# Optimization experiments

Measured on AMD Instinct MI355X. Metric: run time of the kernel, lower is better.

Reference implementation:

```python
import jax, jax.numpy as jnp
import numpy as np

SEQ, EMBED, H, QLR, KVLR, RD, VD = 4096, 2048, 16, 512, 512, 64, 128
KD = VD + RD  # full key/query head dim (content + rope)


def _make_rotary_pe(seq_len, dim):
    inv_freq = 1.0 / jnp.power(10000.0, jnp.arange(0, dim, 2) / dim)
    t = jnp.arange(seq_len)
    freqs = jnp.outer(t, inv_freq)  # (seq, dim//2)
    return jnp.sin(freqs), jnp.cos(freqs)


def _apply_rope(x, sin, cos):
    # x: (seq, ..., dim); sin/cos: (seq, dim//2)
    d = x.shape[-1] // 2
    x1, x2 = x[..., :d], x[..., d:]
    sin2 = jnp.concatenate([sin, sin], axis=-1)
    cos2 = jnp.concatenate([cos, cos], axis=-1)
    ne = x.ndim - 2
    sin2 = sin2.reshape(sin2.shape[0], *[1] * ne, sin2.shape[1])
    cos2 = cos2.reshape(cos2.shape[0], *[1] * ne, cos2.shape[1])
    rot = jnp.concatenate([-x2, x1], axis=-1)
    return x * cos2 + rot * sin2


def setup_inputs() -> dict:
    key = jax.random.key(0)
    ks = jax.random.split(key, 8)

    def w(k, out_dim, in_dim):
        return jax.random.normal(k, (out_dim, in_dim), dtype=jnp.float32) * (1.0 / np.sqrt(in_dim))

    x = jax.random.normal(ks[0], (SEQ, EMBED), dtype=jnp.float32)
    mask = jnp.tril(jnp.ones((SEQ, SEQ), dtype=bool))  # causal
    return {
        "x": x,
        "mask": mask,
        "w_q_down": w(ks[1], QLR, EMBED),
        "w_q_up": w(ks[2], H * VD, QLR),
        "w_q_rope": w(ks[3], H * RD, QLR),
        "w_kv_down": w(ks[4], KVLR, EMBED),
        "w_kv_up": w(ks[5], H * 2 * VD, KVLR),
        "w_k_rope": w(ks[6], RD, EMBED),
        "w_out": w(ks[7], EMBED, H * VD),
    }


def reference(x, mask, w_q_down, w_q_up, w_q_rope, w_kv_down, w_kv_up, w_k_rope, w_out):
    seq = x.shape[0]
    # query path through low-rank bottleneck
    c_q = x @ w_q_down.T                                   # (S, QLR)
    q_content = (c_q @ w_q_up.T).reshape(seq, H, VD)       # (S, H, VD)
    q_rope = (c_q @ w_q_rope.T).reshape(seq, H, RD)        # (S, H, RD)
    # kv path through shared low-rank bottleneck
    c_kv = x @ w_kv_down.T                                 # (S, KVLR)
    kv = c_kv @ w_kv_up.T                                  # (S, H*2*VD)
    k_content_flat, v_flat = jnp.split(kv, 2, axis=-1)
    k_content = k_content_flat.reshape(seq, H, VD)
    v = v_flat.reshape(seq, H, VD)
    # shared rope key (one per token, broadcast to heads)
    k_rope_shared = (x @ w_k_rope.T)[:, None, :]           # (S, 1, RD)
    sin, cos = _make_rotary_pe(seq, RD)
    q_rope_rot = _apply_rope(q_rope, sin, cos)             # (S, H, RD)
    k_rope_rot = jnp.tile(_apply_rope(k_rope_shared, sin, cos), (1, H, 1))
    q_final = jnp.concatenate([q_content, q_rope_rot], axis=-1)  # (S, H, KD)
    k_final = jnp.concatenate([k_content, k_rope_rot], axis=-1)  # (S, H, KD)
    # values zero-padded to key dim
    v_padded = jnp.concatenate(
        [v, jnp.zeros((seq, H, RD), dtype=v.dtype)], axis=-1)    # (S, H, KD)
    # scaled dot-product attention per head
    scale = 1.0 / jnp.sqrt(jnp.asarray(KD, dtype=x.dtype))
    scores = jnp.einsum("shd,thd->hst", q_final, k_final) * scale  # (H, S, S)
    scores = jnp.where(mask[None, :, :], scores, jnp.asarray(-1e9, dtype=scores.dtype))
    probs = jax.nn.softmax(scores, axis=-1)
    attn = jnp.einsum("hst,thd->shd", probs, v_padded)             # (S, H, KD)
    attn = attn[..., :VD].reshape(seq, H * VD)                     # drop zero-pad dims
    return attn @ w_out.T                                          # (S, EMBED)
```

## Files before the change

### kernel.cpp

```cpp
#include <hip/hip_runtime.h>


#define SEQ   4096
#define EMBED 2048
#define NHEAD 16
#define QLR   512
#define KVLR  512
#define RD    64
#define VD    128
#define KDIM  192

typedef __attribute__((ext_vector_type(8)))  _Float16 half8;
typedef __attribute__((ext_vector_type(4)))  _Float16 half4;
typedef __attribute__((ext_vector_type(4)))  float    f32x4;
typedef __attribute__((ext_vector_type(16))) float    f32x16;
typedef __attribute__((ext_vector_type(2)))  unsigned int uint2v;
typedef __attribute__((ext_vector_type(4)))  unsigned int uint4v;

__device__ __forceinline__ void gload16(void* lds, const void* g) {
    __builtin_amdgcn_global_load_lds(
        (const __attribute__((address_space(1))) void*)g,
        (__attribute__((address_space(3))) void*)lds, 16, 0, 0);
}

__device__ __forceinline__ unsigned int pkh(float a, float b) {
    auto h = __builtin_amdgcn_cvt_pkrtz(a, b);
    return __builtin_bit_cast(unsigned int, h);
}

__global__ __launch_bounds__(256) void cvt_plain(const float* __restrict__ s,
                                                 _Float16* __restrict__ d, int n8) {
    const int i = blockIdx.x * 256 + threadIdx.x;
    if (i >= n8) return;
    const float4 a = reinterpret_cast<const float4*>(s)[i * 2];
    const float4 b = reinterpret_cast<const float4*>(s)[i * 2 + 1];
    half8 r;
    r[0] = (_Float16)a.x; r[1] = (_Float16)a.y; r[2] = (_Float16)a.z; r[3] = (_Float16)a.w;
    r[4] = (_Float16)b.x; r[5] = (_Float16)b.y; r[6] = (_Float16)b.z; r[7] = (_Float16)b.w;
    reinterpret_cast<half8*>(d)[i] = r;
}

__global__ __launch_bounds__(256) void cvt_down(const float* __restrict__ wqd,
                                                const float* __restrict__ wkvd,
                                                const float* __restrict__ wkr,
                                                _Float16* __restrict__ dst) {
    const int i = blockIdx.x * 256 + threadIdx.x;
    if (i >= 1152 * 2048 / 8) return;
    const int e = i * 8, row = e >> 11, col = e & 2047;
    const float* src = row < 512  ? wqd  + (size_t)row * 2048 + col
                     : row < 1024 ? wkvd + (size_t)(row - 512) * 2048 + col
                     : row < 1088 ? wkr  + (size_t)(row - 1024) * 2048 + col
                                  : nullptr;
    half8 r = {};
    if (src) {
        const float4 a = reinterpret_cast<const float4*>(src)[0];
        const float4 b = reinterpret_cast<const float4*>(src)[1];
        r[0] = (_Float16)a.x; r[1] = (_Float16)a.y; r[2] = (_Float16)a.z; r[3] = (_Float16)a.w;
        r[4] = (_Float16)b.x; r[5] = (_Float16)b.y; r[6] = (_Float16)b.z; r[7] = (_Float16)b.w;
    }
    reinterpret_cast<half8*>(dst)[i] = r;
}

__global__ __launch_bounds__(256) void cvt_qup(const float* __restrict__ wqu,
                                               const float* __restrict__ wqr,
                                               _Float16* __restrict__ dst) {
    const int i = blockIdx.x * 256 + threadIdx.x;
    if (i >= 3072 * 512 / 8) return;
    const int e = i * 8, row = e >> 9, col = e & 511;
    const float* src = row < 2048 ? wqu + (size_t)row * 512 + col
                                  : wqr + (size_t)(row - 2048) * 512 + col;
    const float4 a = reinterpret_cast<const float4*>(src)[0];
    const float4 b = reinterpret_cast<const float4*>(src)[1];
    half8 r;
    r[0] = (_Float16)a.x; r[1] = (_Float16)a.y; r[2] = (_Float16)a.z; r[3] = (_Float16)a.w;
    r[4] = (_Float16)b.x; r[5] = (_Float16)b.y; r[6] = (_Float16)b.z; r[7] = (_Float16)b.w;
    reinterpret_cast<half8*>(dst)[i] = r;
}

template <int EPI>
__global__ __launch_bounds__(256) void gemm_f16(const _Float16* __restrict__ A,
                                                const _Float16* __restrict__ B,
                                                _Float16* __restrict__ o0,
                                                _Float16* __restrict__ o1,
                                                _Float16* __restrict__ o2,
                                                float* __restrict__ of,
                                                int M, int N, int K)
{
    __shared__ _Float16 sA[128 * 64];
    __shared__ _Float16 sB[128 * 64];

    const int tid  = threadIdx.x;
    const int wid  = tid >> 6;
    const int lane = tid & 63;
    const int lr   = lane & 15;
    const int lg   = lane >> 4;
    const int row0 = blockIdx.y * 128;
    const int col0 = blockIdx.x * 128;
    const int war  = (wid >> 1) * 64;
    const int wac  = (wid & 1) * 64;

    const int sr = lane >> 3;
    const int sk = (lane & 7) * 8;
    const _Float16* Ab = A + (size_t)(row0 + wid * 8 + sr) * K + sk;
    const _Float16* Bb = B + (size_t)(col0 + wid * 8 + sr) * K + sk;

    f32x4 acc[4][4] = {};

    for (int k0 = 0; k0 < K; k0 += 64) {
#pragma unroll
        for (int i = 0; i < 4; ++i) {
            const int c = i * 4 + wid;
            gload16((char*)sA + c * 1024, Ab + (size_t)i * 32 * K + k0);
            gload16((char*)sB + c * 1024, Bb + (size_t)i * 32 * K + k0);
        }
        __syncthreads();

#pragma unroll
        for (int kk = 0; kk < 64; kk += 32) {
            half8 a[4], b[4];
#pragma unroll
            for (int i = 0; i < 4; ++i)
                a[i] = *reinterpret_cast<const half8*>(&sA[(war + i * 16 + lr) * 64 + kk + lg * 8]);
#pragma unroll
            for (int j = 0; j < 4; ++j)
                b[j] = *reinterpret_cast<const half8*>(&sB[(wac + j * 16 + lr) * 64 + kk + lg * 8]);
            __builtin_amdgcn_s_setprio(1);
#pragma unroll
            for (int i = 0; i < 4; ++i)
#pragma unroll
                for (int j = 0; j < 4; ++j)
                    acc[i][j] = __builtin_amdgcn_mfma_f32_16x16x32_f16(a[i], b[j], acc[i][j], 0, 0, 0);
            __builtin_amdgcn_s_setprio(0);
        }
        __syncthreads();
    }

#pragma unroll
    for (int i = 0; i < 4; ++i)
#pragma unroll
        for (int j = 0; j < 4; ++j) {
            const int grow0 = row0 + war + i * 16 + lg * 4;
            const int gcol  = col0 + wac + j * 16 + lr;
            if constexpr (EPI == 2) {
                if (gcol >= 2048) {
                    half4 pv;
#pragma unroll
                    for (int r = 0; r < 4; ++r) pv[r] = (_Float16)acc[i][j][r];
                    *reinterpret_cast<half4*>(&o1[(size_t)(gcol - 2048) * SEQ + grow0]) = pv;
                    continue;
                }
            }
#pragma unroll
            for (int r = 0; r < 4; ++r) {
                const int grow = grow0 + r;
                const float v = acc[i][j][r];
                if constexpr (EPI == 0) {
                    if (gcol < 512)       o0[(size_t)grow * 512 + gcol] = (_Float16)v;
                    else if (gcol < 1024) o1[(size_t)grow * 512 + gcol - 512] = (_Float16)v;
                    else if (gcol < 1088) o2[(size_t)grow * 64 + gcol - 1024] = (_Float16)v;
                } else if constexpr (EPI == 1) {
                    if (gcol < 2048)
                        o0[(size_t)grow * (NHEAD * KDIM) + (gcol >> 7) * KDIM + (gcol & 127)] = (_Float16)v;
                    else {
                        const int c = gcol - 2048;
                        o0[(size_t)grow * (NHEAD * KDIM) + (c >> 6) * KDIM + VD + (c & 63)] = (_Float16)v;
                    }
                } else if constexpr (EPI == 2) {
                    o0[((size_t)(gcol >> 7) * SEQ + grow) * KDIM + (gcol & 127)] = (_Float16)v;
                } else {
                    of[(size_t)grow * N + gcol] = v;
                }
            }
        }
}

__global__ __launch_bounds__(256) void rope_kernel(_Float16* __restrict__ qf,
                                                   _Float16* __restrict__ kf,
                                                   const _Float16* __restrict__ ktmp)
{
    __shared__ float s_sin[32], s_cos[32];
    const int s   = blockIdx.x;
    const int tid = threadIdx.x;
    if (tid < 32) {
        const double inv = exp(-(double)tid * (log(10000.0) / 32.0));
        const double ang = (double)s * inv;
        s_sin[tid] = (float)sin(ang);
        s_cos[tid] = (float)cos(ang);
    }
    __syncthreads();

    for (int p = tid; p < NHEAD * 32; p += 256) {
        const int h = p >> 5, i = p & 31;
        const size_t base = (size_t)s * (NHEAD * KDIM) + h * KDIM + VD;
        const float x1 = (float)qf[base + i];
        const float x2 = (float)qf[base + 32 + i];
        const float cs = s_cos[i], sn = s_sin[i];
        qf[base + i]      = (_Float16)(x1 * cs - x2 * sn);
        qf[base + 32 + i] = (_Float16)(x2 * cs + x1 * sn);
    }
    if (tid < 32) {
        const int i = tid;
        const float x1 = (float)ktmp[(size_t)s * RD + i];
        const float x2 = (float)ktmp[(size_t)s * RD + 32 + i];
        const float cs = s_cos[i], sn = s_sin[i];
        const _Float16 r1 = (_Float16)(x1 * cs - x2 * sn);
        const _Float16 r2 = (_Float16)(x2 * cs + x1 * sn);
#pragma unroll
        for (int h = 0; h < NHEAD; ++h) {
            const size_t base = ((size_t)h * SEQ + s) * KDIM + VD;
            kf[base + i]      = r1;
            kf[base + 32 + i] = r2;
        }
    }
}

__global__ __launch_bounds__(256, 2) void fattn(const _Float16* __restrict__ qf,
                                                const _Float16* __restrict__ kf,
                                                const _Float16* __restrict__ vT,
                                                _Float16* __restrict__ attn)
{
    __shared__ _Float16 sK[2][64 * 192];
    __shared__ _Float16 sV[128 * 64];

    const int idx = blockIdx.x;
    const int h   = idx & 15;
    const int qt  = 31 - (idx >> 4);
    const int q0  = qt * 128;

    const int tid  = threadIdx.x;
    const int wid  = tid >> 6;
    const int lane = tid & 63;
    const int l31  = lane & 31;
    const int h5   = lane >> 5;
    const int x7   = l31 & 7;
    const int qg   = q0 + wid * 32 + l31;
    const int q0w  = q0 + wid * 32;

    const float scale = 0.0721687836487032f;

    const _Float16* ksrc[6];
    int klds[6];
#pragma unroll
    for (int i = 0; i < 6; ++i) {
        const int c   = wid * 6 + i;
        const int gi  = c * 64 + lane;
        const int row = gi / 24;
        const int g   = gi % 24;
        ksrc[i] = kf + ((size_t)h * SEQ + row) * KDIM + ((g ^ (row & 7)) << 3);
        klds[i] = c * 1024;
    }
    const _Float16* vsrc[4];
    int vlds[4];
#pragma unroll
    for (int i = 0; i < 4; ++i) {
        const int c = wid * 4 + i;
        const int d = c * 8 + (lane >> 3);
        vsrc[i] = vT + ((size_t)h * VD + d) * SEQ + (((lane & 7) ^ (lane >> 3)) << 3);
        vlds[i] = c * 1024;
    }

    half8 qfr[12];
    {
        const _Float16* qb_ = qf + (size_t)qg * (NHEAD * KDIM) + h * KDIM + h5 * 8;
#pragma unroll
        for (int ks = 0; ks < 12; ++ks)
            qfr[ks] = *reinterpret_cast<const half8*>(qb_ + ks * 16);
    }

    f32x16 o0 = {}, o1 = {}, o2 = {}, o3 = {};
    float m_ = -1e30f, l_ = 0.0f;

    const int nt = 2 * qt + 2;

    {
#pragma unroll
        for (int i = 0; i < 6; ++i) gload16((char*)sK[0] + klds[i], ksrc[i]);
#pragma unroll
        for (int i = 0; i < 4; ++i) gload16((char*)sV + vlds[i], vsrc[i]);
    }
    __syncthreads();

    int cur = 0;
    for (int t = 0; t < nt; ++t) {
        const int j0 = t * 64;

        if (t + 1 < nt) {
            const size_t joff = (size_t)(j0 + 64) * KDIM;
#pragma unroll
            for (int i = 0; i < 6; ++i)
                gload16((char*)sK[cur ^ 1] + klds[i], ksrc[i] + joff);
        }

        f32x16 s0 = {}, s1 = {};
        {
            const char* kb = (const char*)sK[cur];
            __builtin_amdgcn_s_setprio(1);
#pragma unroll
            for (int ks = 0; ks < 12; ++ks) {
                const int go = ((ks * 2 + h5) ^ x7) << 4;
                const half8 ka = *reinterpret_cast<const half8*>(kb + l31 * 384 + go);
                const half8 kc = *reinterpret_cast<const half8*>(kb + (32 + l31) * 384 + go);
                s0 = __builtin_amdgcn_mfma_f32_32x32x16_f16(ka, qfr[ks], s0, 0, 0, 0);
                s1 = __builtin_amdgcn_mfma_f32_32x32x16_f16(kc, qfr[ks], s1, 0, 0, 0);
            }
            __builtin_amdgcn_s_setprio(0);
        }

#pragma unroll
        for (int m = 0; m < 16; ++m) { s0[m] *= scale; s1[m] *= scale; }
        if (j0 + 63 > q0w) {
#pragma unroll
            for (int m = 0; m < 16; ++m) {
                const int kv = j0 + (m & 3) + 8 * (m >> 2) + 4 * h5;
                if (kv > qg)      s0[m] = -3.0e38f;
                if (kv + 32 > qg) s1[m] = -3.0e38f;
            }
        }

        float mx = s0[0];
#pragma unroll
        for (int m = 1; m < 16; ++m) mx = fmaxf(mx, s0[m]);
#pragma unroll
        for (int m = 0; m < 16; ++m) mx = fmaxf(mx, s1[m]);
        mx = fmaxf(mx, __shfl_xor(mx, 32, 64));

        if (!__all(mx - m_ <= 8.0f)) {
            const float mn = fmaxf(m_, mx);
            const float alpha = __expf(m_ - mn);
            m_ = mn;
            l_ *= alpha;
#pragma unroll
            for (int m = 0; m < 16; ++m) {
                o0[m] *= alpha; o1[m] *= alpha; o2[m] *= alpha; o3[m] *= alpha;
            }
        }
        float rs = 0.0f;
#pragma unroll
        for (int m = 0; m < 16; ++m) { const float p = __expf(s0[m] - m_); s0[m] = p; rs += p; }
#pragma unroll
        for (int m = 0; m < 16; ++m) { const float p = __expf(s1[m] - m_); s1[m] = p; rs += p; }
        rs += __shfl_xor(rs, 32, 64);
        l_ += rs;

        half8 pb0, pb1, pb2, pb3;
        {
            unsigned int x, x2, y, y2;
            x  = pkh(s0[0], s0[1]);  x2 = pkh(s0[2], s0[3]);
            y  = pkh(s0[4], s0[5]);  y2 = pkh(s0[6], s0[7]);
            uint2v r1 = __builtin_amdgcn_permlane32_swap(x, y, false, false);
            uint2v r2 = __builtin_amdgcn_permlane32_swap(x2, y2, false, false);
            { uint4v u = { r1[0], r2[0], r1[1], r2[1] }; pb0 = __builtin_bit_cast(half8, u); }
            x  = pkh(s0[8], s0[9]);  x2 = pkh(s0[10], s0[11]);
            y  = pkh(s0[12], s0[13]); y2 = pkh(s0[14], s0[15]);
            r1 = __builtin_amdgcn_permlane32_swap(x, y, false, false);
            r2 = __builtin_amdgcn_permlane32_swap(x2, y2, false, false);
            { uint4v u = { r1[0], r2[0], r1[1], r2[1] }; pb1 = __builtin_bit_cast(half8, u); }
            x  = pkh(s1[0], s1[1]);  x2 = pkh(s1[2], s1[3]);
            y  = pkh(s1[4], s1[5]);  y2 = pkh(s1[6], s1[7]);
            r1 = __builtin_amdgcn_permlane32_swap(x, y, false, false);
            r2 = __builtin_amdgcn_permlane32_swap(x2, y2, false, false);
            { uint4v u = { r1[0], r2[0], r1[1], r2[1] }; pb2 = __builtin_bit_cast(half8, u); }
            x  = pkh(s1[8], s1[9]);  x2 = pkh(s1[10], s1[11]);
            y  = pkh(s1[12], s1[13]); y2 = pkh(s1[14], s1[15]);
            r1 = __builtin_amdgcn_permlane32_swap(x, y, false, false);
            r2 = __builtin_amdgcn_permlane32_swap(x2, y2, false, false);
            { uint4v u = { r1[0], r2[0], r1[1], r2[1] }; pb3 = __builtin_bit_cast(half8, u); }
        }

        __syncthreads();

        {
            const char* vbse = (const char*)sV;
            __builtin_amdgcn_s_setprio(1);
#pragma unroll
            for (int ks = 0; ks < 4; ++ks) {
                const int go = ((ks * 2 + h5) ^ x7) << 4;
                const half8 pbk = ks == 0 ? pb0 : ks == 1 ? pb1 : ks == 2 ? pb2 : pb3;
                const half8 v0 = *reinterpret_cast<const half8*>(vbse + (l31)      * 128 + go);
                const half8 v1 = *reinterpret_cast<const half8*>(vbse + (32 + l31) * 128 + go);
                const half8 v2 = *reinterpret_cast<const half8*>(vbse + (64 + l31) * 128 + go);
                const half8 v3 = *reinterpret_cast<const half8*>(vbse + (96 + l31) * 128 + go);
                o0 = __builtin_amdgcn_mfma_f32_32x32x16_f16(v0, pbk, o0, 0, 0, 0);
                o1 = __builtin_amdgcn_mfma_f32_32x32x16_f16(v1, pbk, o1, 0, 0, 0);
                o2 = __builtin_amdgcn_mfma_f32_32x32x16_f16(v2, pbk, o2, 0, 0, 0);
                o3 = __builtin_amdgcn_mfma_f32_32x32x16_f16(v3, pbk, o3, 0, 0, 0);
            }
            __builtin_amdgcn_s_setprio(0);
        }

        __syncthreads();

        if (t + 1 < nt) {
            const int jn = j0 + 64;
#pragma unroll
            for (int i = 0; i < 4; ++i)
                gload16((char*)sV + vlds[i], vsrc[i] + jn);
        }
        cur ^= 1;
    }

    const float invl = 1.0f / l_;
    _Float16* ob = attn + (size_t)qg * (NHEAD * VD) + h * VD + 4 * h5;
#pragma unroll
    for (int g = 0; g < 4; ++g) {
#pragma unroll
        for (int pp = 0; pp < 2; ++pp) {
            const int m = g * 4 + pp * 2;
            const int dof = pp * 2 + 8 * g;
            *reinterpret_cast<unsigned int*>(ob + dof) =
                pkh(o0[m] * invl, o0[m + 1] * invl);
            *reinterpret_cast<unsigned int*>(ob + 32 + dof) =
                pkh(o1[m] * invl, o1[m + 1] * invl);
            *reinterpret_cast<unsigned int*>(ob + 64 + dof) =
                pkh(o2[m] * invl, o2[m + 1] * invl);
            *reinterpret_cast<unsigned int*>(ob + 96 + dof) =
                pkh(o3[m] * invl, o3[m + 1] * invl);
        }
    }
}

extern "C" void kernel_launch(void* const* d_in, const int* in_sizes, int n_in,
                              void* d_out, int out_size, void* d_ws, size_t ws_size,
                              hipStream_t stream)
{
    (void)in_sizes; (void)n_in; (void)out_size; (void)ws_size;
    const float* x    = (const float*)d_in[0];
    const float* wqd  = (const float*)d_in[2];
    const float* wqu  = (const float*)d_in[3];
    const float* wqr  = (const float*)d_in[4];
    const float* wkvd = (const float*)d_in[5];
    const float* wkvu = (const float*)d_in[6];
    const float* wkr  = (const float*)d_in[7];
    const float* wout = (const float*)d_in[8];
    float* out = (float*)d_out;

    char* ws = (char*)d_ws;
    _Float16* x_h    = (_Float16*)ws; ws += (size_t)SEQ * EMBED * 2;
    _Float16* wdownh = (_Float16*)ws; ws += (size_t)1152 * EMBED * 2;
    _Float16* wquph  = (_Float16*)ws; ws += (size_t)3072 * QLR * 2;
    _Float16* wkvuh  = (_Float16*)ws; ws += (size_t)4096 * KVLR * 2;
    _Float16* c_q    = (_Float16*)ws; ws += (size_t)SEQ * QLR * 2;
    _Float16* c_kv   = (_Float16*)ws; ws += (size_t)SEQ * KVLR * 2;
    _Float16* ktmp   = (_Float16*)ws; ws += (size_t)SEQ * RD * 2;
    _Float16* qfin   = (_Float16*)ws; ws += (size_t)SEQ * NHEAD * KDIM * 2;
    _Float16* kfin   = (_Float16*)ws; ws += (size_t)SEQ * NHEAD * KDIM * 2;
    _Float16* vT     = (_Float16*)ws; ws += (size_t)NHEAD * VD * SEQ * 2;
    _Float16* attn   = x_h;
    _Float16* wouth  = c_q;

    dim3 blk(256);

    cvt_plain<<<dim3(4096), blk, 0, stream>>>(x, x_h, SEQ * EMBED / 8);
    cvt_down <<<dim3(1152), blk, 0, stream>>>(wqd, wkvd, wkr, wdownh);
    cvt_qup  <<<dim3(768),  blk, 0, stream>>>(wqu, wqr, wquph);
    cvt_plain<<<dim3(1024), blk, 0, stream>>>(wkvu, wkvuh, 4096 * KVLR / 8);

    gemm_f16<0><<<dim3(9, 32), blk, 0, stream>>>(
        x_h, wdownh, c_q, c_kv, ktmp, nullptr, SEQ, 1152, EMBED);
    gemm_f16<1><<<dim3(24, 32), blk, 0, stream>>>(
        c_q, wquph, qfin, nullptr, nullptr, nullptr, SEQ, 3072, QLR);
    gemm_f16<2><<<dim3(32, 32), blk, 0, stream>>>(
        c_kv, wkvuh, kfin, vT, nullptr, nullptr, SEQ, 4096, KVLR);

    cvt_plain<<<dim3(2048), blk, 0, stream>>>(wout, wouth, EMBED * EMBED / 8);

    rope_kernel<<<dim3(SEQ), blk, 0, stream>>>(qfin, kfin, ktmp);
    fattn<<<dim3(512), blk, 0, stream>>>(qfin, kfin, vT, attn);
    gemm_f16<3><<<dim3(16, 32), blk, 0, stream>>>(
        attn, wouth, nullptr, nullptr, nullptr, out, SEQ, EMBED, NHEAD * VD);
}
```

Measured before the change: 335.1 us.

## Load V fragments directly from global memory instead of staging through LDS

Removes the shared-memory V buffer and its async global-to-LDS copies, and has each wave read its V^T MFMA operands straight from global memory into registers. The loads are interleaved with the PV MFMAs in a two-buffer register rotation. One of the two barriers per KV tile goes away and LDS use drops, which may allow higher occupancy. In exchange, every wave of a block now reads the same V tile from global/L2 (4x redundant traffic), and load latency is exposed inside the loop with no cross-iteration prefetch.

```diff
diff --git a/kernel.cpp b/kernel.cpp
--- a/kernel.cpp
+++ b/kernel.cpp
@@ -220,7 +220,6 @@
                                                 _Float16* __restrict__ attn)
 {
     __shared__ _Float16 sK[2][64 * 192];
-    __shared__ _Float16 sV[128 * 64];
 
     const int idx = blockIdx.x;
     const int h   = idx & 15;
@@ -249,15 +248,8 @@
         ksrc[i] = kf + ((size_t)h * SEQ + row) * KDIM + ((g ^ (row & 7)) << 3);
         klds[i] = c * 1024;
     }
-    const _Float16* vsrc[4];
-    int vlds[4];
-#pragma unroll
-    for (int i = 0; i < 4; ++i) {
-        const int c = wid * 4 + i;
-        const int d = c * 8 + (lane >> 3);
-        vsrc[i] = vT + ((size_t)h * VD + d) * SEQ + (((lane & 7) ^ (lane >> 3)) << 3);
-        vlds[i] = c * 1024;
-    }
+
+    const _Float16* vb = vT + ((size_t)h * VD + l31) * SEQ + h5 * 8;
 
     half8 qfr[12];
     {
@@ -272,12 +264,8 @@
 
     const int nt = 2 * qt + 2;
 
-    {
-#pragma unroll
-        for (int i = 0; i < 6; ++i) gload16((char*)sK[0] + klds[i], ksrc[i]);
-#pragma unroll
-        for (int i = 0; i < 4; ++i) gload16((char*)sV + vlds[i], vsrc[i]);
-    }
+#pragma unroll
+    for (int i = 0; i < 6; ++i) gload16((char*)sK[0] + klds[i], ksrc[i]);
     __syncthreads();
 
     int cur = 0;
@@ -305,6 +293,11 @@
             }
             __builtin_amdgcn_s_setprio(0);
         }
+
+        half8 vfA[4], vfB[4];
+#pragma unroll
+        for (int ks = 0; ks < 4; ++ks)
+            vfA[ks] = *reinterpret_cast<const half8*>(vb + j0 + ks * 16);
 
 #pragma unroll
         for (int m = 0; m < 16; ++m) { s0[m] *= scale; s1[m] *= scale; }
@@ -367,35 +360,35 @@
             { uint4v u = { r1[0], r2[0], r1[1], r2[1] }; pb3 = __builtin_bit_cast(half8, u); }
         }
 
+        __builtin_amdgcn_s_setprio(1);
+#pragma unroll
+        for (int ks = 0; ks < 4; ++ks)
+            vfB[ks] = *reinterpret_cast<const half8*>(vb + 32 * SEQ + j0 + ks * 16);
+        o0 = __builtin_amdgcn_mfma_f32_32x32x16_f16(vfA[0], pb0, o0, 0, 0, 0);
+        o0 = __builtin_amdgcn_mfma_f32_32x32x16_f16(vfA[1], pb1, o0, 0, 0, 0);
+        o0 = __builtin_amdgcn_mfma_f32_32x32x16_f16(vfA[2], pb2, o0, 0, 0, 0);
+        o0 = __builtin_amdgcn_mfma_f32_32x32x16_f16(vfA[3], pb3, o0, 0, 0, 0);
+#pragma unroll
+        for (int ks = 0; ks < 4; ++ks)
+            vfA[ks] = *reinterpret_cast<const half8*>(vb + 64 * SEQ + j0 + ks * 16);
+        o1 = __builtin_amdgcn_mfma_f32_32x32x16_f16(vfB[0], pb0, o1, 0, 0, 0);
+        o1 = __builtin_amdgcn_mfma_f32_32x32x16_f16(vfB[1], pb1, o1, 0, 0, 0);
+        o1 = __builtin_amdgcn_mfma_f32_32x32x16_f16(vfB[2], pb2, o1, 0, 0, 0);
+        o1 = __builtin_amdgcn_mfma_f32_32x32x16_f16(vfB[3], pb3, o1, 0, 0, 0);
+#pragma unroll
+        for (int ks = 0; ks < 4; ++ks)
+            vfB[ks] = *reinterpret_cast<const half8*>(vb + 96 * SEQ + j0 + ks * 16);
+        o2 = __builtin_amdgcn_mfma_f32_32x32x16_f16(vfA[0], pb0, o2, 0, 0, 0);
+        o2 = __builtin_amdgcn_mfma_f32_32x32x16_f16(vfA[1], pb1, o2, 0, 0, 0);
+        o2 = __builtin_amdgcn_mfma_f32_32x32x16_f16(vfA[2], pb2, o2, 0, 0, 0);
+        o2 = __builtin_amdgcn_mfma_f32_32x32x16_f16(vfA[3], pb3, o2, 0, 0, 0);
+        o3 = __builtin_amdgcn_mfma_f32_32x32x16_f16(vfB[0], pb0, o3, 0, 0, 0);
+        o3 = __builtin_amdgcn_mfma_f32_32x32x16_f16(vfB[1], pb1, o3, 0, 0, 0);
+        o3 = __builtin_amdgcn_mfma_f32_32x32x16_f16(vfB[2], pb2, o3, 0, 0, 0);
+        o3 = __builtin_amdgcn_mfma_f32_32x32x16_f16(vfB[3], pb3, o3, 0, 0, 0);
+        __builtin_amdgcn_s_setprio(0);
+
         __syncthreads();
-
-        {
-            const char* vbse = (const char*)sV;
-            __builtin_amdgcn_s_setprio(1);
-#pragma unroll
-            for (int ks = 0; ks < 4; ++ks) {
-                const int go = ((ks * 2 + h5) ^ x7) << 4;
-                const half8 pbk = ks == 0 ? pb0 : ks == 1 ? pb1 : ks == 2 ? pb2 : pb3;
-                const half8 v0 = *reinterpret_cast<const half8*>(vbse + (l31)      * 128 + go);
-                const half8 v1 = *reinterpret_cast<const half8*>(vbse + (32 + l31) * 128 + go);
-                const half8 v2 = *reinterpret_cast<const half8*>(vbse + (64 + l31) * 128 + go);
-                const half8 v3 = *reinterpret_cast<const half8*>(vbse + (96 + l31) * 128 + go);
-                o0 = __builtin_amdgcn_mfma_f32_32x32x16_f16(v0, pbk, o0, 0, 0, 0);
-                o1 = __builtin_amdgcn_mfma_f32_32x32x16_f16(v1, pbk, o1, 0, 0, 0);
-                o2 = __builtin_amdgcn_mfma_f32_32x32x16_f16(v2, pbk, o2, 0, 0, 0);
-                o3 = __builtin_amdgcn_mfma_f32_32x32x16_f16(v3, pbk, o3, 0, 0, 0);
-            }
-            __builtin_amdgcn_s_setprio(0);
-        }
-
-        __syncthreads();
-
-        if (t + 1 < nt) {
-            const int jn = j0 + 64;
-#pragma unroll
-            for (int i = 0; i < 4; ++i)
-                gload16((char*)sV + vlds[i], vsrc[i] + jn);
-        }
         cur ^= 1;
     }
 
```

Result: slower. 431.0 us (+28.6%).

## Double-buffer V tiles, fold softmax scale into Q, use exp2 softmax

Applied to the files above, without the earlier changes.

Gives the V tile its own double buffer, so the next V tile is prefetched together with the next K tile. This removes one of the two per-iteration block barriers. It also folds the attention scale times log2(e) into the Q projection epilogue and switches the softmax to exp2f, which drops the per-score multiply. The max and sum reductions are split into independent chains, and the lazy-rescale threshold is widened to match the base-2 domain. LDS use per block rises to about 80KB. The fp16 Q values are now pre-scaled, which slightly changes rounding.

```diff
diff --git a/kernel.cpp b/kernel.cpp
--- a/kernel.cpp
+++ b/kernel.cpp
@@ -9,6 +9,8 @@
 #define RD    64
 #define VD    128
 #define KDIM  192
+
+#define QSCALE 0.104121521f
 
 typedef __attribute__((ext_vector_type(8)))  _Float16 half8;
 typedef __attribute__((ext_vector_type(4)))  _Float16 half4;
@@ -159,11 +161,12 @@
                     else if (gcol < 1024) o1[(size_t)grow * 512 + gcol - 512] = (_Float16)v;
                     else if (gcol < 1088) o2[(size_t)grow * 64 + gcol - 1024] = (_Float16)v;
                 } else if constexpr (EPI == 1) {
+                    const float vs = v * QSCALE;
                     if (gcol < 2048)
-                        o0[(size_t)grow * (NHEAD * KDIM) + (gcol >> 7) * KDIM + (gcol & 127)] = (_Float16)v;
+                        o0[(size_t)grow * (NHEAD * KDIM) + (gcol >> 7) * KDIM + (gcol & 127)] = (_Float16)vs;
                     else {
                         const int c = gcol - 2048;
-                        o0[(size_t)grow * (NHEAD * KDIM) + (c >> 6) * KDIM + VD + (c & 63)] = (_Float16)v;
+                        o0[(size_t)grow * (NHEAD * KDIM) + (c >> 6) * KDIM + VD + (c & 63)] = (_Float16)vs;
                     }
                 } else if constexpr (EPI == 2) {
                     o0[((size_t)(gcol >> 7) * SEQ + grow) * KDIM + (gcol & 127)] = (_Float16)v;
@@ -220,7 +223,7 @@
                                                 _Float16* __restrict__ attn)
 {
     __shared__ _Float16 sK[2][64 * 192];
-    __shared__ _Float16 sV[128 * 64];
+    __shared__ _Float16 sV[2][128 * 64];
 
     const int idx = blockIdx.x;
     const int h   = idx & 15;
@@ -236,8 +239,6 @@
     const int qg   = q0 + wid * 32 + l31;
     const int q0w  = q0 + wid * 32;
 
-    const float scale = 0.0721687836487032f;
-
     const _Float16* ksrc[6];
     int klds[6];
 #pragma unroll
@@ -272,12 +273,10 @@
 
     const int nt = 2 * qt + 2;
 
-    {
-#pragma unroll
-        for (int i = 0; i < 6; ++i) gload16((char*)sK[0] + klds[i], ksrc[i]);
-#pragma unroll
-        for (int i = 0; i < 4; ++i) gload16((char*)sV + vlds[i], vsrc[i]);
-    }
+#pragma unroll
+    for (int i = 0; i < 6; ++i) gload16((char*)sK[0] + klds[i], ksrc[i]);
+#pragma unroll
+    for (int i = 0; i < 4; ++i) gload16((char*)sV[0] + vlds[i], vsrc[i]);
     __syncthreads();
 
     int cur = 0;
@@ -289,6 +288,9 @@
 #pragma unroll
             for (int i = 0; i < 6; ++i)
                 gload16((char*)sK[cur ^ 1] + klds[i], ksrc[i] + joff);
+#pragma unroll
+            for (int i = 0; i < 4; ++i)
+                gload16((char*)sV[cur ^ 1] + vlds[i], vsrc[i] + j0 + 64);
         }
 
         f32x16 s0 = {}, s1 = {};
@@ -306,8 +308,6 @@
             __builtin_amdgcn_s_setprio(0);
         }
 
-#pragma unroll
-        for (int m = 0; m < 16; ++m) { s0[m] *= scale; s1[m] *= scale; }
         if (j0 + 63 > q0w) {
 #pragma unroll
             for (int m = 0; m < 16; ++m) {
@@ -317,16 +317,19 @@
             }
         }
 
-        float mx = s0[0];
-#pragma unroll
-        for (int m = 1; m < 16; ++m) mx = fmaxf(mx, s0[m]);
-#pragma unroll
-        for (int m = 0; m < 16; ++m) mx = fmaxf(mx, s1[m]);
+        float ma = fmaxf(s0[0], s0[1]);
+        float mb = fmaxf(s1[0], s1[1]);
+#pragma unroll
+        for (int m = 2; m < 16; m += 2) {
+            ma = fmaxf(fmaxf(ma, s0[m]), s0[m + 1]);
+            mb = fmaxf(fmaxf(mb, s1[m]), s1[m + 1]);
+        }
+        float mx = fmaxf(ma, mb);
         mx = fmaxf(mx, __shfl_xor(mx, 32, 64));
 
-        if (!__all(mx - m_ <= 8.0f)) {
+        if (!__all(mx - m_ <= 11.5f)) {
             const float mn = fmaxf(m_, mx);
-            const float alpha = __expf(m_ - mn);
+            const float alpha = exp2f(m_ - mn);
             m_ = mn;
             l_ *= alpha;
 #pragma unroll
@@ -334,11 +337,15 @@
                 o0[m] *= alpha; o1[m] *= alpha; o2[m] *= alpha; o3[m] *= alpha;
             }
         }
-        float rs = 0.0f;
-#pragma unroll
-        for (int m = 0; m < 16; ++m) { const float p = __expf(s0[m] - m_); s0[m] = p; rs += p; }
-#pragma unroll
-        for (int m = 0; m < 16; ++m) { const float p = __expf(s1[m] - m_); s1[m] = p; rs += p; }
+        float ra = 0.0f, rb = 0.0f, rc = 0.0f, rd = 0.0f;
+#pragma unroll
+        for (int m = 0; m < 16; m += 2) {
+            const float pa = exp2f(s0[m] - m_);     s0[m] = pa;     ra += pa;
+            const float pc = exp2f(s0[m + 1] - m_); s0[m + 1] = pc; rb += pc;
+            const float pe = exp2f(s1[m] - m_);     s1[m] = pe;     rc += pe;
+            const float pg = exp2f(s1[m + 1] - m_); s1[m + 1] = pg; rd += pg;
+        }
+        float rs = (ra + rb) + (rc + rd);
         rs += __shfl_xor(rs, 32, 64);
         l_ += rs;
 
@@ -367,10 +374,8 @@
             { uint4v u = { r1[0], r2[0], r1[1], r2[1] }; pb3 = __builtin_bit_cast(half8, u); }
         }
 
-        __syncthreads();
-
         {
-            const char* vbse = (const char*)sV;
+            const char* vbse = (const char*)sV[cur];
             __builtin_amdgcn_s_setprio(1);
 #pragma unroll
             for (int ks = 0; ks < 4; ++ks) {
@@ -389,13 +394,6 @@
         }
 
         __syncthreads();
-
-        if (t + 1 < nt) {
-            const int jn = j0 + 64;
-#pragma unroll
-            for (int i = 0; i < 4; ++i)
-                gload16((char*)sV + vlds[i], vsrc[i] + jn);
-        }
         cur ^= 1;
     }
 
```

Measured after the change: 346.9 us. 3.5% more time.
